# Optimization experiments

Measured on AMD Instinct MI355X. Metric: run time of the kernel, lower is better.

Reference implementation:

```python
import jax, jax.numpy as jnp
import numpy as np
import math

# geometry: ROI [-140.8,-40,-3,140.8,40,1], grid 0.4 -> (Z,Y,X)=(10,200,704)
B_AG = 2              # total agents = 1 sample x 2 agents
Z, Y, X = 10, 200, 704
Z1, Y1, X1 = 5, 100, 352   # after stride-2 conv (k=3, p=1)
N_PTS = 10000         # active radar voxels per agent
C_IN, C0, C1 = 64, 32, 64
N_IN = B_AG * N_PTS
CAP0 = 27 * N_IN                # padded bound on spconv0 active outputs
CAP1 = B_AG * Z1 * Y1 * X1      # padded bound on spconv1 active outputs
EPS = 1e-5

_OFFS = np.array([[a, b, c] for a in range(3) for b in range(3) for c in range(3)])


def _spconv_rulebook(coords, stride, zyx, pair_cap, out_cap):
    """Rulebook for SparseConv3d k=3 pad=1. coords [N,4]=(b,z,y,x).
    Returns gather [27,P], scatter [27,P] (dummy=out_cap), out coords padded
    to out_cap (pad coords are out-of-bounds so dense scatter drops them)."""
    oz, oy, ox = zyx
    per_in, per_lin = [], []
    for off in _OFFS:
        t = coords[:, 1:] + 1 - off
        ok = (t % stride == 0).all(1)
        o = t // stride
        ok &= (o >= 0).all(1) & (o[:, 0] < oz) & (o[:, 1] < oy) & (o[:, 2] < ox)
        idx = np.nonzero(ok)[0]
        oc = o[idx]
        per_in.append(idx)
        per_lin.append(((coords[idx, 0] * oz + oc[:, 0]) * oy + oc[:, 1]) * ox + oc[:, 2])
    all_lin = np.unique(np.concatenate(per_lin))
    n_out = len(all_lin)
    g = np.zeros((27, pair_cap), np.int32)
    s = np.full((27, pair_cap), out_cap, np.int32)
    for k in range(27):
        n = len(per_in[k])
        g[k, :n] = per_in[k]
        s[k, :n] = np.searchsorted(all_lin, per_lin[k])
    b = all_lin // (oz * oy * ox); r = all_lin % (oz * oy * ox)
    zc = r // (oy * ox); r = r % (oy * ox)
    out_coords = np.stack([b, zc, r // ox, r % ox], 1).astype(np.int32)
    pad = np.zeros((out_cap - n_out, 4), np.int32); pad[:, 1] = oz  # OOB -> dropped
    return g, s, np.concatenate([out_coords, pad], 0), n_out


def _subm_rulebook(coords, n_act, zyx, pair_cap, out_cap):
    """SubMConv3d k=3: same active set in/out; coords[:n_act] sorted by lin id."""
    oz, oy, ox = zyx
    c = coords[:n_act]
    lins = ((c[:, 0] * oz + c[:, 1]) * oy + c[:, 2]) * ox + c[:, 3]
    g = np.zeros((27, pair_cap), np.int32)
    s = np.full((27, pair_cap), out_cap, np.int32)
    for k, off in enumerate(_OFFS):
        cand = c[:, 1:] + (off - 1)
        ok = (cand >= 0).all(1) & (cand[:, 0] < oz) & (cand[:, 1] < oy) & (cand[:, 2] < ox)
        cl = ((c[:, 0] * oz + cand[:, 0]) * oy + cand[:, 1]) * ox + cand[:, 2]
        pos = np.minimum(np.searchsorted(lins, cl), n_act - 1)
        ok &= lins[pos] == cl
        idx = np.nonzero(ok)[0]
        g[k, :len(idx)] = pos[idx]
        s[k, :len(idx)] = idx
    return g, s


def setup_inputs() -> dict:
    rng = np.random.default_rng(0)
    cl = []
    for b in range(B_AG):
        lin = np.sort(rng.choice(Z * Y * X, N_PTS, replace=False))
        z = lin // (Y * X); r = lin % (Y * X)
        cl.append(np.stack([np.full(N_PTS, b), z, r // X, r % X], 1))
    coords_in = np.concatenate(cl, 0).astype(np.int64)

    g0, s0, coords0, n0 = _spconv_rulebook(coords_in, 1, (Z, Y, X), N_IN, CAP0)
    ga, sa = _subm_rulebook(coords0, n0, (Z, Y, X), CAP0, CAP0)
    g1, s1, coords1, n1 = _spconv_rulebook(coords0[:n0], 2, (Z1, Y1, X1), CAP0, CAP1)
    gb, sb = _subm_rulebook(coords1, n1, (Z1, Y1, X1), CAP1, CAP1)

    ks = jax.random.split(jax.random.key(0), 20)
    f32 = jnp.float32
    def W(k, *shape, fan):
        return jax.random.normal(k, shape, f32) * (1.0 / np.sqrt(fan))
    def bn(k, c):  # [gamma, beta, running_mean, running_var]
        m = jax.random.normal(k, (c,), f32) * 0.1
        v = 1.0 + jax.random.uniform(jax.random.fold_in(k, 1), (c,), f32)
        return jnp.stack([jnp.ones((c,), f32), jnp.zeros((c,), f32), m, v])
    return dict(
        sp_feats=jax.random.normal(ks[0], (N_IN, C_IN), f32),
        w_in=W(ks[1], C_IN, C0, fan=C_IN),
        w0=W(ks[2], 27, C0, C0, fan=27 * C0), bnp0=bn(ks[3], C0),
        w0a=W(ks[4], 27, C0, C0, fan=27 * C0), bnp0a=bn(ks[5], C0),
        w0b=W(ks[6], 27, C0, C0, fan=27 * C0), bnp0b=bn(ks[7], C0),
        w1=W(ks[8], 27, C0, C1, fan=27 * C0), bnp1=bn(ks[9], C1),
        w1a=W(ks[10], 27, C1, C1, fan=27 * C1), bnp1a=bn(ks[11], C1),
        w1b=W(ks[12], 27, C1, C1, fan=27 * C1), bnp1b=bn(ks[13], C1),
        ct0_w=W(ks[14], C0 * Z, 64, 1, 1, fan=C0 * Z), ct0_b=jnp.zeros((64,), f32),
        bnt0=bn(ks[15], 64),
        ct1_w=W(ks[16], C1 * Z1, 64, 2, 2, fan=C1 * Z1 * 4), ct1_b=jnp.zeros((64,), f32),
        bnt1=bn(ks[17], 64),
        coords0=jnp.asarray(coords0), coords1=jnp.asarray(coords1),
        g0=jnp.asarray(g0), s0=jnp.asarray(s0),
        ga=jnp.asarray(ga), sa=jnp.asarray(sa),
        g1=jnp.asarray(g1), s1=jnp.asarray(s1),
        gb=jnp.asarray(gb), sb=jnp.asarray(sb),
        record_len=2,
    )


def _bn1d(x, p):  # x [N,C]; p [4,C]
    g, b, m, v = p
    return (x - m) * (g * jax.lax.rsqrt(v + EPS)) + b


def _bn2d(x, p):  # x [B,C,H,W]
    g, b, m, v = (t[:, None, None] for t in p)
    return (x - m) * (g * jax.lax.rsqrt(v + EPS)) + b


def _spconv(feats, g, s, W, out_cap):
    """gather-GEMM-scatter: feats [Nin,Cin], g/s [27,P], W [27,Cin,Cout]."""
    out = jnp.zeros((out_cap + 1, W.shape[2]), feats.dtype)  # +1 dummy row
    for k in range(27):
        out = out.at[s[k]].add(feats[g[k]] @ W[k])
    return out[:out_cap]


def _to_dense(feats, coords, b, z, y, x):
    d = jnp.zeros((b, z, y, x, feats.shape[1]), feats.dtype)
    d = d.at[coords[:, 0], coords[:, 1], coords[:, 2], coords[:, 3]].add(feats)
    return d.transpose(0, 4, 1, 2, 3)  # B,C,Z,Y,X


def _conv_t2d(x, w, b, stride, pad):
    """torch ConvTranspose2d; w [Cin,Cout,k,k]."""
    k = w.shape[2]
    wf = jnp.flip(w, (2, 3)).transpose(1, 0, 2, 3)  # Cout,Cin,k,k
    out = jax.lax.conv_general_dilated(
        x, wf, window_strides=(1, 1),
        padding=[(k - 1 - pad, k - 1 - pad)] * 2,
        lhs_dilation=(stride, stride),
        dimension_numbers=('NCHW', 'OIHW', 'NCHW'))
    return out + b[None, :, None, None]


def _att_fusion(x, L):
    """OpenCOOD AttFusion: per-pixel scaled dot-product attention over agents,
    keep ego (agent 0). Assumes uniform record_len == L."""
    B, C, H, Wd = x.shape
    S = B // L
    xr = x.reshape(S, L, C, H * Wd).transpose(0, 3, 1, 2)  # S,HW,L,C
    att = jax.nn.softmax(jnp.einsum('snlc,snmc->snlm', xr, xr) / math.sqrt(C), -1)
    h = jnp.einsum('snlm,snmc->snlc', att, xr)[:, :, 0, :]  # ego agent
    return h.transpose(0, 2, 1).reshape(S, C, H, Wd)


def reference(sp_feats, w_in, w0, bnp0, w0a, bnp0a, w0b, bnp0b,
              w1, bnp1, w1a, bnp1a, w1b, bnp1b,
              ct0_w, ct0_b, bnt0, ct1_w, ct1_b, bnt1,
              coords0, coords1, g0, s0, ga, sa, g1, s1, gb, sb, record_len):
    relu = jax.nn.relu
    f = sp_feats @ w_in                         # input_conv (k=1)
    # ---- encoder layer 0 (stride 1) ----
    f = relu(_bn1d(_spconv(f, g0, s0, w0, CAP0), bnp0))
    f = relu(_bn1d(_spconv(f, ga, sa, w0a, CAP0), bnp0a))
    f = relu(_bn1d(_spconv(f, ga, sa, w0b, CAP0), bnp0b))
    d0 = _to_dense(f, coords0, B_AG, Z, Y, X).reshape(B_AG, C0 * Z, Y, X)  # b (c z) y x
    bev0 = relu(_bn2d(_conv_t2d(d0, ct0_w, ct0_b, 1, 0), bnt0))
    bev0 = _att_fusion(bev0, record_len)
    # ---- encoder layer 1 (stride 2) ----
    f = relu(_bn1d(_spconv(f, g1, s1, w1, CAP1), bnp1))
    f = relu(_bn1d(_spconv(f, gb, sb, w1a, CAP1), bnp1a))
    f = relu(_bn1d(_spconv(f, gb, sb, w1b, CAP1), bnp1b))
    d1 = _to_dense(f, coords1, B_AG, Z1, Y1, X1).reshape(B_AG, C1 * Z1, Y1, X1)
    bev1 = relu(_bn2d(_conv_t2d(d1, ct1_w, ct1_b, 2, 0), bnt1))
    bev1 = _att_fusion(bev1, record_len)
    return jnp.concatenate([bev0, bev1], axis=1)  # [S, 128, 200, 704]
```

## Files before the change

kernel.cpp:

```cpp
#include <hip/hip_runtime.h>
#include <hip/hip_bf16.h>
#include <hip/hip_fp16.h>

#define N_PTS_IN   20000
#define CAP0C      540000
#define CAP1C      352000
#define ZD 10
#define YD 200
#define XD 704
#define Z1D 5
#define Y1D 100
#define X1D 352
#define HWOUT (YD*XD)

typedef _Float16 f16x8 __attribute__((ext_vector_type(8)));
typedef float    f32x4 __attribute__((ext_vector_type(4)));

__global__ __launch_bounds__(256) void gemm_in(const float* __restrict__ sp,
                                               const float* __restrict__ w,
                                               __half* __restrict__ fout) {
    int tid = blockIdx.x * 256 + threadIdx.x;
    int row = tid >> 3;
    int c4  = (tid & 7) * 4;
    if (row >= N_PTS_IN) return;
    float4 acc = {0.f, 0.f, 0.f, 0.f};
    const float* sr = sp + (size_t)row * 64;
#pragma unroll
    for (int ci = 0; ci < 64; ci += 4) {
        float4 fv = *(const float4*)(sr + ci);
        const float* wp = w + ci * 32 + c4;
        float4 w0 = *(const float4*)(wp);
        float4 w1 = *(const float4*)(wp + 32);
        float4 w2 = *(const float4*)(wp + 64);
        float4 w3 = *(const float4*)(wp + 96);
        acc.x += fv.x*w0.x + fv.y*w1.x + fv.z*w2.x + fv.w*w3.x;
        acc.y += fv.x*w0.y + fv.y*w1.y + fv.z*w2.y + fv.w*w3.y;
        acc.z += fv.x*w0.z + fv.y*w1.z + fv.z*w2.z + fv.w*w3.z;
        acc.w += fv.x*w0.w + fv.y*w1.w + fv.z*w2.w + fv.w*w3.w;
    }
    __half* fo = fout + (size_t)row * 32 + c4;
    fo[0] = __float2half(acc.x);
    fo[1] = __float2half(acc.y);
    fo[2] = __float2half(acc.z);
    fo[3] = __float2half(acc.w);
}

__global__ __launch_bounds__(256) void cvt_w(const float* __restrict__ src,
                                             __half* __restrict__ dst,
                                             int CIN, int COUT) {
    int i = blockIdx.x * 256 + threadIdx.x;
    if (i >= 27 * CIN * COUT) return;
    int ci = i % CIN;
    int t  = i / CIN;
    int co = t % COUT;
    int k  = t / COUT;
    dst[i] = __float2half(src[((size_t)k * CIN + ci) * COUT + co]);
}

__global__ __launch_bounds__(256) void cvt_ct0(const float* __restrict__ src,
                                               __half* __restrict__ dst) {
    int i = blockIdx.x * 256 + threadIdx.x;
    if (i >= 64 * 320) return;
    int zc = i % 320, co = i / 320;
    int z = zc >> 5, c = zc & 31;
    dst[i] = __float2half(src[(c * 10 + z) * 64 + co]);
}

__global__ __launch_bounds__(256) void cvt_ct1(const float* __restrict__ src,
                                               __half* __restrict__ dst) {
    int i = blockIdx.x * 256 + threadIdx.x;
    if (i >= 4 * 64 * 320) return;
    int zc = i % 320;
    int t  = i / 320;
    int co = t & 63;
    int kq = t >> 6;
    int z = zc >> 6, c = zc & 63;
    dst[i] = __float2half(src[((c * 5 + z) * 64 + co) * 4 + kq]);
}

__global__ __launch_bounds__(256) void build_nbr(const int* __restrict__ g,
                                                 const int* __restrict__ s,
                                                 int* __restrict__ nbrT,
                                                 int P, int cap) {
    int i = blockIdx.x * 256 + threadIdx.x;
    if (i >= 27 * P) return;
    int k = i / P, p = i - k * P;
    int sv = s[(size_t)k * P + p];
    if (sv >= cap) return;
    nbrT[(size_t)k * cap + sv] = g[(size_t)k * P + p];
}

__global__ __launch_bounds__(128) void find_nact(const int* __restrict__ c0,
                                                 const int* __restrict__ c1,
                                                 int* __restrict__ nA) {
    int t = threadIdx.x;
    if (t == 0) {
        int lo = 0, hi = CAP0C;
        while (lo < hi) {
            int mid = (lo + hi) >> 1;
            if (c0[4 * mid + 1] >= ZD) hi = mid; else lo = mid + 1;
        }
        nA[0] = lo;
    } else if (t == 64) {
        int lo = 0, hi = CAP1C;
        while (lo < hi) {
            int mid = (lo + hi) >> 1;
            if (c1[4 * mid + 1] >= Z1D) hi = mid; else lo = mid + 1;
        }
        nA[1] = lo;
    }
}

__global__ __launch_bounds__(256) void build_vox(const int* __restrict__ coords,
                                                 int* __restrict__ v2r,
                                                 int cap, int Zdim, int Ydim, int Xdim) {
    int r = blockIdx.x * 256 + threadIdx.x;
    if (r >= cap) return;
    int b = coords[4*r], z = coords[4*r+1], y = coords[4*r+2], x = coords[4*r+3];
    if (z >= Zdim) return;
    v2r[(((size_t)b * Zdim + z) * Ydim + y) * Xdim + x] = r;
}

template <int CIN, int COUT>
__global__ __launch_bounds__(256) void spconv_reg(const __half* __restrict__ f,
                                                  const __half* __restrict__ wt,
                                                  const float* __restrict__ bnp,
                                                  const int* __restrict__ nbrT,
                                                  __half* __restrict__ fout,
                                                  int ncap,
                                                  const int* __restrict__ nA) {
    constexpr int NT = COUT / 16;
    constexpr int KT = CIN / 32;
    constexpr int NCHUNK = CIN / 8;
    constexpr int MASK = NCHUNK - 1;
    constexpr int LCH  = (NCHUNK == 8) ? 3 : 2;
    constexpr int TILE_H = COUT * CIN;
    constexpr int TB = TILE_H * 2 / 256;
    constexpr int OST_H = 4 * 32 * COUT;
    constexpr int SH_H = (2 * TILE_H > OST_H) ? 2 * TILE_H : OST_H;
    __shared__ __align__(16) __half S[SH_H];

    int tid = threadIdx.x;
    int wv = tid >> 6, lane = tid & 63;
    int quad = lane >> 4, l16 = lane & 15;

    int bid = blockIdx.x;
    int nfull = (int)gridDim.x & ~63;
    int sb;
    if (bid < nfull) {
        int grp = bid >> 6, w = bid & 63;
        sb = grp * 64 + (w & 7) * 8 + (w >> 3);
    } else {
        sb = bid;
    }

    if (sb * 128 >= *nA) return;

    int m0 = sb * 128 + wv * 32;
    int r0 = m0 + l16;
    int r1 = m0 + 16 + l16;
    bool ok0 = r0 < ncap, ok1 = r1 < ncap;

    f32x4 acc[2][NT] = {};

    int gC0 = ok0 ? nbrT[r0] : -1;
    int gC1 = ok1 ? nbrT[r1] : -1;
    int gN0 = ok0 ? nbrT[(size_t)ncap + r0] : -1;
    int gN1 = ok1 ? nbrT[(size_t)ncap + r1] : -1;
    bool ever = false;

    {
        const char* src = (const char*)(wt) + tid * TB;
        if constexpr (TB == 32) {
            uint4 w0 = *(const uint4*)src;
            uint4 w1 = *(const uint4*)(src + 16);
            int p0 = tid * 2;
#pragma unroll
            for (int j = 0; j < 2; ++j) {
                int p = p0 + j;
                int row = p >> LCH, c = p & MASK;
                *(uint4*)(S + (row * NCHUNK + (c ^ (row & MASK))) * 8) = (j ? w1 : w0);
            }
        } else if constexpr (TB == 16) {
            uint4 w0 = *(const uint4*)src;
            int p = tid;
            int row = p >> LCH, c = p & MASK;
            *(uint4*)(S + (row * NCHUNK + (c ^ (row & MASK))) * 8) = w0;
        } else {
            uint2 w0 = *(const uint2*)src;
            int p = tid >> 1, half = tid & 1;
            int row = p >> LCH, c = p & MASK;
            *(uint2*)(S + (row * NCHUNK + (c ^ (row & MASK))) * 8 + half * 4) = w0;
        }
    }
    __syncthreads();

#pragma unroll 1
    for (int k = 0; k < 27; ++k) {
        int gNN0 = -1, gNN1 = -1;
        if (k + 2 < 27) {
            if (ok0) gNN0 = nbrT[(size_t)(k + 2) * ncap + r0];
            if (ok1) gNN1 = nbrT[(size_t)(k + 2) * ncap + r1];
        }
        bool anyC = __ballot((gC0 >= 0) || (gC1 >= 0)) != 0ull;
        f16x8 a0[KT], a1[KT];
        if (anyC) {
            const __half* p0 = f + (size_t)((gC0 < 0) ? 0 : gC0) * CIN + quad * 8;
            const __half* p1 = f + (size_t)((gC1 < 0) ? 0 : gC1) * CIN + quad * 8;
#pragma unroll
            for (int kt = 0; kt < KT; ++kt) {
                uint4 u0 = {0u,0u,0u,0u}, u1 = {0u,0u,0u,0u};
                if (gC0 >= 0) u0 = *(const uint4*)(p0 + kt * 32);
                if (gC1 >= 0) u1 = *(const uint4*)(p1 + kt * 32);
                a0[kt] = *(f16x8*)&u0;
                a1[kt] = *(f16x8*)&u1;
            }
        }
        bool doStage = (k + 1 < 27);
        uint4 w0{}, w1{}; uint2 w2{};
        if (doStage) {
            const char* src = (const char*)(wt + (size_t)(k + 1) * TILE_H) + tid * TB;
            if constexpr (TB == 32)      { w0 = *(const uint4*)src; w1 = *(const uint4*)(src + 16); }
            else if constexpr (TB == 16) { w0 = *(const uint4*)src; }
            else                         { w2 = *(const uint2*)src; }
        }
        if (anyC) {
            ever = true;
            const __half* Wb = S + (k & 1) * TILE_H;
#pragma unroll
            for (int kt = 0; kt < KT; ++kt) {
#pragma unroll
                for (int nt = 0; nt < NT; ++nt) {
                    int row = nt * 16 + l16;
                    int c   = kt * 4 + quad;
                    f16x8 b = *(const f16x8*)(Wb + (row * NCHUNK + (c ^ (row & MASK))) * 8);
                    acc[0][nt] = __builtin_amdgcn_mfma_f32_16x16x32_f16(a0[kt], b, acc[0][nt], 0, 0, 0);
                    acc[1][nt] = __builtin_amdgcn_mfma_f32_16x16x32_f16(a1[kt], b, acc[1][nt], 0, 0, 0);
                }
            }
        }
        if (doStage) {
            __half* dst = S + ((k + 1) & 1) * TILE_H;
            if constexpr (TB == 32) {
                int p0 = tid * 2;
#pragma unroll
                for (int j = 0; j < 2; ++j) {
                    int p = p0 + j;
                    int row = p >> LCH, c = p & MASK;
                    *(uint4*)(dst + (row * NCHUNK + (c ^ (row & MASK))) * 8) = (j ? w1 : w0);
                }
            } else if constexpr (TB == 16) {
                int p = tid;
                int row = p >> LCH, c = p & MASK;
                *(uint4*)(dst + (row * NCHUNK + (c ^ (row & MASK))) * 8) = w0;
            } else {
                int p = tid >> 1, half = tid & 1;
                int row = p >> LCH, c = p & MASK;
                *(uint2*)(dst + (row * NCHUNK + (c ^ (row & MASK))) * 8 + half * 4) = w2;
            }
        }
        __syncthreads();
        gC0 = gN0; gC1 = gN1; gN0 = gNN0; gN1 = gNN1;
    }

    if (!ever) return;
    __half* O = S + wv * (32 * COUT);
#pragma unroll
    for (int nt = 0; nt < NT; ++nt) {
        int co = nt * 16 + l16;
        float g = bnp[co], b = bnp[COUT + co];
        float mn = bnp[2*COUT + co], vv = bnp[3*COUT + co];
        float s  = g * rsqrtf(vv + 1e-5f);
        float sh = b - mn * s;
#pragma unroll
        for (int m = 0; m < 2; ++m)
#pragma unroll
            for (int r_ = 0; r_ < 4; ++r_) {
                int row = m * 16 + quad * 4 + r_;
                O[row * COUT + co] = __float2half(fmaxf(acc[m][nt][r_] * s + sh, 0.f));
            }
    }
    constexpr int OCH = COUT / 8;
#pragma unroll
    for (int j = 0; j < 32 * OCH / 64; ++j) {
        int idx = j * 64 + lane;
        int r = idx / OCH, c = idx % OCH;
        if (m0 + r < ncap)
            *(uint4*)(fout + (size_t)(m0 + r) * COUT + c * 8) =
                *(const uint4*)(O + r * COUT + c * 8);
    }
}

__global__ __launch_bounds__(256) void bev0_mfma(const __half* __restrict__ f0,
                                                 const __half* __restrict__ wtT,
                                                 const float* __restrict__ bias,
                                                 const float* __restrict__ bnp,
                                                 const int* __restrict__ v2r,
                                                 float* __restrict__ out) {
    constexpr int AST = 328;
    __shared__ __align__(16) __half Al[64 * AST];
    __shared__ float Cl[64][65];
    __shared__ float Ot[64][33];
    int tid = threadIdx.x;
    int y = blockIdx.x / 22, x0 = (blockIdx.x % 22) * 32;
    int wv = tid >> 6, lane = tid & 63;
    int quad = lane >> 4, l16 = lane & 15;

    for (int it = 0; it < 3; ++it) {
        int task = it * 256 + tid;
        if (task < 640) {
            int row = task & 63, z = task >> 6;
            int b = row & 1, p = row >> 1;
            int r = v2r[((b * ZD + z) * YD + y) * XD + x0 + p];
            uint4 v0 = {0,0,0,0}, v1 = {0,0,0,0}, v2 = {0,0,0,0}, v3 = {0,0,0,0};
            if (r >= 0) {
                const uint4* src = (const uint4*)(f0 + (size_t)r * 32);
                v0 = src[0]; v1 = src[1]; v2 = src[2]; v3 = src[3];
            }
            uint4* dst = (uint4*)(Al + row * AST + z * 32);
            dst[0] = v0; dst[1] = v1; dst[2] = v2; dst[3] = v3;
        }
    }
    __syncthreads();

    f32x4 acc[4] = {};
#pragma unroll
    for (int ks = 0; ks < 10; ++ks) {
        f16x8 a = *(const f16x8*)(Al + (wv * 16 + l16) * AST + ks * 32 + quad * 8);
#pragma unroll
        for (int nt = 0; nt < 4; ++nt) {
            f16x8 bfr = *(const f16x8*)(wtT + (size_t)(nt * 16 + l16) * 320 + ks * 32 + quad * 8);
            acc[nt] = __builtin_amdgcn_mfma_f32_16x16x32_f16(a, bfr, acc[nt], 0, 0, 0);
        }
    }
#pragma unroll
    for (int nt = 0; nt < 4; ++nt) {
        int co = nt * 16 + l16;
        float s  = bnp[co] * rsqrtf(bnp[192 + co] + 1e-5f);
        float sh = (bias[co] - bnp[128 + co]) * s + bnp[64 + co];
#pragma unroll
        for (int r_ = 0; r_ < 4; ++r_)
            Cl[wv * 16 + quad * 4 + r_][co] = fmaxf(acc[nt][r_] * s + sh, 0.f);
    }
#pragma unroll
    for (int pi = 0; pi < 8; ++pi) {
        int p = wv * 8 + pi;
        float x0v = Cl[2 * p][lane], x1v = Cl[2 * p + 1][lane];
        float s00 = x0v * x0v, s01 = x0v * x1v;
#pragma unroll
        for (int o = 32; o > 0; o >>= 1) {
            s00 += __shfl_xor(s00, o);
            s01 += __shfl_xor(s01, o);
        }
        float a0 = s00 * 0.125f, a1 = s01 * 0.125f;
        float mx = fmaxf(a0, a1);
        float e0 = expf(a0 - mx), e1 = expf(a1 - mx);
        float inv = 1.f / (e0 + e1);
        Ot[lane][p] = (e0 * x0v + e1 * x1v) * inv;
    }
    __syncthreads();
#pragma unroll
    for (int i = 0; i < 8; ++i) {
        int idx = i * 256 + tid;
        int co = idx >> 5, px = idx & 31;
        out[(size_t)co * HWOUT + (size_t)y * XD + x0 + px] = Ot[co][px];
    }
}

__global__ __launch_bounds__(256) void bev1_mfma(const __half* __restrict__ f1,
                                                 const __half* __restrict__ wtT,
                                                 const float* __restrict__ bias,
                                                 const float* __restrict__ bnp,
                                                 const int* __restrict__ v2r,
                                                 float* __restrict__ out) {
    constexpr int AST = 328;
    __shared__ __align__(16) __half Al[64 * AST];
    __shared__ float Cl[64][65];
    __shared__ float Ot[64][65];
    int tid = threadIdx.x;
    int iy = blockIdx.x / 11, j0 = (blockIdx.x % 11) * 32;
    int wv = tid >> 6, lane = tid & 63;
    int quad = lane >> 4, l16 = lane & 15;

    for (int it = 0; it < 3; ++it) {
        int task = it * 256 + tid;
        if (task < 640) {
            int row = task & 63, zh = task >> 6;
            int z = zh >> 1, hf = zh & 1;
            int b = row & 1, p = row >> 1;
            int r = v2r[((b * Z1D + z) * Y1D + iy) * X1D + j0 + p];
            uint4 v0 = {0,0,0,0}, v1 = {0,0,0,0}, v2 = {0,0,0,0}, v3 = {0,0,0,0};
            if (r >= 0) {
                const uint4* src = (const uint4*)(f1 + (size_t)r * 64 + hf * 32);
                v0 = src[0]; v1 = src[1]; v2 = src[2]; v3 = src[3];
            }
            uint4* dst = (uint4*)(Al + row * AST + z * 64 + hf * 32);
            dst[0] = v0; dst[1] = v1; dst[2] = v2; dst[3] = v3;
        }
    }
    __syncthreads();

#pragma unroll 1
    for (int ky = 0; ky < 2; ++ky) {
#pragma unroll 1
        for (int kx = 0; kx < 2; ++kx) {
            const __half* wk = wtT + (size_t)(ky * 2 + kx) * 64 * 320;
            f32x4 acc[4] = {};
#pragma unroll
            for (int ks = 0; ks < 10; ++ks) {
                f16x8 a = *(const f16x8*)(Al + (wv * 16 + l16) * AST + ks * 32 + quad * 8);
#pragma unroll
                for (int nt = 0; nt < 4; ++nt) {
                    f16x8 bfr = *(const f16x8*)(wk + (size_t)(nt * 16 + l16) * 320 + ks * 32 + quad * 8);
                    acc[nt] = __builtin_amdgcn_mfma_f32_16x16x32_f16(a, bfr, acc[nt], 0, 0, 0);
                }
            }
#pragma unroll
            for (int nt = 0; nt < 4; ++nt) {
                int co = nt * 16 + l16;
                float s  = bnp[co] * rsqrtf(bnp[192 + co] + 1e-5f);
                float sh = (bias[co] - bnp[128 + co]) * s + bnp[64 + co];
#pragma unroll
                for (int r_ = 0; r_ < 4; ++r_)
                    Cl[wv * 16 + quad * 4 + r_][co] = fmaxf(acc[nt][r_] * s + sh, 0.f);
            }
#pragma unroll
            for (int pi = 0; pi < 8; ++pi) {
                int p = wv * 8 + pi;
                float x0v = Cl[2 * p][lane], x1v = Cl[2 * p + 1][lane];
                float s00 = x0v * x0v, s01 = x0v * x1v;
#pragma unroll
                for (int o = 32; o > 0; o >>= 1) {
                    s00 += __shfl_xor(s00, o);
                    s01 += __shfl_xor(s01, o);
                }
                float a0 = s00 * 0.125f, a1 = s01 * 0.125f;
                float mx = fmaxf(a0, a1);
                float e0 = expf(a0 - mx), e1 = expf(a1 - mx);
                float inv = 1.f / (e0 + e1);
                Ot[lane][2 * p + kx] = (e0 * x0v + e1 * x1v) * inv;
            }
        }
        __syncthreads();
        int yo = 2 * iy + ky;
#pragma unroll
        for (int i = 0; i < 16; ++i) {
            int idx = i * 256 + tid;
            int co = idx >> 6, xx = idx & 63;
            out[(size_t)co * HWOUT + (size_t)yo * XD + 2 * j0 + xx] = Ot[co][xx];
        }
        __syncthreads();
    }
}

extern "C" void kernel_launch(void* const* d_in, const int* in_sizes, int n_in,
                              void* d_out, int out_size, void* d_ws, size_t ws_size,
                              hipStream_t stream) {
    const float* sp    = (const float*)d_in[0];
    const float* w_in  = (const float*)d_in[1];
    const float* w0    = (const float*)d_in[2];
    const float* bnp0  = (const float*)d_in[3];
    const float* w0a   = (const float*)d_in[4];
    const float* bnp0a = (const float*)d_in[5];
    const float* w0b   = (const float*)d_in[6];
    const float* bnp0b = (const float*)d_in[7];
    const float* w1    = (const float*)d_in[8];
    const float* bnp1  = (const float*)d_in[9];
    const float* w1a   = (const float*)d_in[10];
    const float* bnp1a = (const float*)d_in[11];
    const float* w1b   = (const float*)d_in[12];
    const float* bnp1b = (const float*)d_in[13];
    const float* ct0w  = (const float*)d_in[14];
    const float* ct0b  = (const float*)d_in[15];
    const float* bnt0  = (const float*)d_in[16];
    const float* ct1w  = (const float*)d_in[17];
    const float* ct1b  = (const float*)d_in[18];
    const float* bnt1  = (const float*)d_in[19];
    const int* coords0 = (const int*)d_in[20];
    const int* coords1 = (const int*)d_in[21];
    const int* g0 = (const int*)d_in[22];
    const int* s0 = (const int*)d_in[23];
    const int* ga = (const int*)d_in[24];
    const int* sa = (const int*)d_in[25];
    const int* g1 = (const int*)d_in[26];
    const int* s1 = (const int*)d_in[27];
    const int* gb = (const int*)d_in[28];
    const int* sb = (const int*)d_in[29];
    float* out = (float*)d_out;

    __half* fInH = (__half*)d_ws;
    __half* R1h  = fInH + 640000;
    __half* R2h  = R1h + 22528000;
    __half* wt0  = R2h + 22528000;
    __half* wt0a = wt0  + 27648;
    __half* wt0b = wt0a + 27648;
    __half* wt1  = wt0b + 27648;
    __half* wt1a = wt1  + 55296;
    __half* wt1b = wt1a + 110592;
    __half* wtT0 = wt1b + 110592;
    __half* wtT1 = wtT0 + 20480;
    int*   nbrT = (int*)(wtT1 + 81920);
    int*   v2r0 = nbrT;
    int*   v2r1 = nbrT + 2816000;
    int*   nAct = nbrT + 14580000;

    find_nact<<<1, 128, 0, stream>>>(coords0, coords1, nAct);
    cvt_w<<<(27*32*32 + 255) / 256, 256, 0, stream>>>(w0,  wt0,  32, 32);
    cvt_w<<<(27*32*32 + 255) / 256, 256, 0, stream>>>(w0a, wt0a, 32, 32);
    cvt_w<<<(27*32*32 + 255) / 256, 256, 0, stream>>>(w0b, wt0b, 32, 32);
    cvt_w<<<(27*32*64 + 255) / 256, 256, 0, stream>>>(w1,  wt1,  32, 64);
    cvt_w<<<(27*64*64 + 255) / 256, 256, 0, stream>>>(w1a, wt1a, 64, 64);
    cvt_w<<<(27*64*64 + 255) / 256, 256, 0, stream>>>(w1b, wt1b, 64, 64);
    cvt_ct0<<<(64*320 + 255) / 256, 256, 0, stream>>>(ct0w, wtT0);
    cvt_ct1<<<(4*64*320 + 255) / 256, 256, 0, stream>>>(ct1w, wtT1);

    gemm_in<<<(N_PTS_IN * 8 + 255) / 256, 256, 0, stream>>>(sp, w_in, fInH);

    hipMemsetAsync(nbrT, 0xFF, (size_t)CAP0C * 27 * 4, stream);
    build_nbr<<<(27 * N_PTS_IN + 255) / 256, 256, 0, stream>>>(g0, s0, nbrT, N_PTS_IN, CAP0C);
    spconv_reg<32, 32><<<(CAP0C + 127) / 128, 256, 0, stream>>>(fInH, wt0, bnp0, nbrT, R1h, CAP0C, nAct + 0);

    hipMemsetAsync(nbrT, 0xFF, (size_t)CAP0C * 27 * 4, stream);
    build_nbr<<<(27 * CAP0C + 255) / 256, 256, 0, stream>>>(ga, sa, nbrT, CAP0C, CAP0C);
    spconv_reg<32, 32><<<(CAP0C + 127) / 128, 256, 0, stream>>>(R1h, wt0a, bnp0a, nbrT, R2h, CAP0C, nAct + 0);
    spconv_reg<32, 32><<<(CAP0C + 127) / 128, 256, 0, stream>>>(R2h, wt0b, bnp0b, nbrT, R1h, CAP0C, nAct + 0);

    hipMemsetAsync(v2r0, 0xFF, (size_t)2816000 * 4, stream);
    build_vox<<<(CAP0C + 255) / 256, 256, 0, stream>>>(coords0, v2r0, CAP0C, ZD, YD, XD);
    bev0_mfma<<<YD * 22, 256, 0, stream>>>(R1h, wtT0, ct0b, bnt0, v2r0, out);

    hipMemsetAsync(nbrT, 0xFF, (size_t)CAP1C * 27 * 4, stream);
    build_nbr<<<(27 * CAP0C + 255) / 256, 256, 0, stream>>>(g1, s1, nbrT, CAP0C, CAP1C);
    spconv_reg<32, 64><<<(CAP1C + 127) / 128, 256, 0, stream>>>(R1h, wt1, bnp1, nbrT, R2h, CAP1C, nAct + 1);

    hipMemsetAsync(nbrT, 0xFF, (size_t)CAP1C * 27 * 4, stream);
    build_nbr<<<(27 * CAP1C + 255) / 256, 256, 0, stream>>>(gb, sb, nbrT, CAP1C, CAP1C);
    spconv_reg<64, 64><<<(CAP1C + 127) / 128, 256, 0, stream>>>(R2h, wt1a, bnp1a, nbrT, R1h, CAP1C, nAct + 1);
    spconv_reg<64, 64><<<(CAP1C + 127) / 128, 256, 0, stream>>>(R1h, wt1b, bnp1b, nbrT, R2h, CAP1C, nAct + 1);

    hipMemsetAsync(v2r1, 0xFF, (size_t)352000 * 4, stream);
    build_vox<<<(CAP1C + 255) / 256, 256, 0, stream>>>(coords1, v2r1, CAP1C, Z1D, Y1D, X1D);
    bev1_mfma<<<Y1D * 11, 256, 0, stream>>>(R2h, wtT1, ct1b, bnt1, v2r1, out + (size_t)64 * HWOUT);
}
```

Baseline: 1.024 ms.

## Load BEV conv A-operands directly into registers and fuse attention in-register

Result: faster. 977.2 us (-4.6%).

```diff
diff --git a/kernel.cpp b/kernel.cpp
--- a/kernel.cpp
+++ b/kernel.cpp
@@ -297,72 +297,85 @@
                                                  const float* __restrict__ bnp,
                                                  const int* __restrict__ v2r,
                                                  float* __restrict__ out) {
-    constexpr int AST = 328;
-    __shared__ __align__(16) __half Al[64 * AST];
-    __shared__ float Cl[64][65];
-    __shared__ float Ot[64][33];
+    __shared__ float Ot[64][66];
     int tid = threadIdx.x;
-    int y = blockIdx.x / 22, x0 = (blockIdx.x % 22) * 32;
+    int y = blockIdx.x / 11, x0 = (blockIdx.x % 11) * 64;
     int wv = tid >> 6, lane = tid & 63;
     int quad = lane >> 4, l16 = lane & 15;
 
-    for (int it = 0; it < 3; ++it) {
-        int task = it * 256 + tid;
-        if (task < 640) {
-            int row = task & 63, z = task >> 6;
-            int b = row & 1, p = row >> 1;
-            int r = v2r[((b * ZD + z) * YD + y) * XD + x0 + p];
-            uint4 v0 = {0,0,0,0}, v1 = {0,0,0,0}, v2 = {0,0,0,0}, v3 = {0,0,0,0};
-            if (r >= 0) {
-                const uint4* src = (const uint4*)(f0 + (size_t)r * 32);
-                v0 = src[0]; v1 = src[1]; v2 = src[2]; v3 = src[3];
-            }
-            uint4* dst = (uint4*)(Al + row * AST + z * 32);
-            dst[0] = v0; dst[1] = v1; dst[2] = v2; dst[3] = v3;
-        }
-    }
-    __syncthreads();
-
-    f32x4 acc[4] = {};
+    int rz[2][10];
+#pragma unroll
+    for (int m = 0; m < 2; ++m) {
+        int row = wv * 32 + m * 16 + l16;
+        int b = row & 1, p = row >> 1;
+#pragma unroll
+        for (int z = 0; z < 10; ++z)
+            rz[m][z] = v2r[((b * ZD + z) * YD + y) * XD + x0 + p];
+    }
+
+    f32x4 acc[2][4] = {};
 #pragma unroll
     for (int ks = 0; ks < 10; ++ks) {
-        f16x8 a = *(const f16x8*)(Al + (wv * 16 + l16) * AST + ks * 32 + quad * 8);
+        f16x8 a[2];
+#pragma unroll
+        for (int m = 0; m < 2; ++m) {
+            uint4 u = {0u,0u,0u,0u};
+            int r = rz[m][ks];
+            if (r >= 0) u = *(const uint4*)(f0 + (size_t)r * 32 + quad * 8);
+            a[m] = *(f16x8*)&u;
+        }
 #pragma unroll
         for (int nt = 0; nt < 4; ++nt) {
-            f16x8 bfr = *(const f16x8*)(wtT + (size_t)(nt * 16 + l16) * 320 + ks * 32 + quad * 8);
-            acc[nt] = __builtin_amdgcn_mfma_f32_16x16x32_f16(a, bfr, acc[nt], 0, 0, 0);
-        }
-    }
+            f16x8 b = *(const f16x8*)(wtT + (size_t)(nt * 16 + l16) * 320 + ks * 32 + quad * 8);
+            acc[0][nt] = __builtin_amdgcn_mfma_f32_16x16x32_f16(a[0], b, acc[0][nt], 0, 0, 0);
+            acc[1][nt] = __builtin_amdgcn_mfma_f32_16x16x32_f16(a[1], b, acc[1][nt], 0, 0, 0);
+        }
+    }
+
 #pragma unroll
     for (int nt = 0; nt < 4; ++nt) {
         int co = nt * 16 + l16;
         float s  = bnp[co] * rsqrtf(bnp[192 + co] + 1e-5f);
         float sh = (bias[co] - bnp[128 + co]) * s + bnp[64 + co];
 #pragma unroll
-        for (int r_ = 0; r_ < 4; ++r_)
-            Cl[wv * 16 + quad * 4 + r_][co] = fmaxf(acc[nt][r_] * s + sh, 0.f);
-    }
-#pragma unroll
-    for (int pi = 0; pi < 8; ++pi) {
-        int p = wv * 8 + pi;
-        float x0v = Cl[2 * p][lane], x1v = Cl[2 * p + 1][lane];
-        float s00 = x0v * x0v, s01 = x0v * x1v;
-#pragma unroll
-        for (int o = 32; o > 0; o >>= 1) {
-            s00 += __shfl_xor(s00, o);
-            s01 += __shfl_xor(s01, o);
-        }
-        float a0 = s00 * 0.125f, a1 = s01 * 0.125f;
-        float mx = fmaxf(a0, a1);
-        float e0 = expf(a0 - mx), e1 = expf(a1 - mx);
-        float inv = 1.f / (e0 + e1);
-        Ot[lane][p] = (e0 * x0v + e1 * x1v) * inv;
-    }
+        for (int m = 0; m < 2; ++m)
+#pragma unroll
+            for (int r_ = 0; r_ < 4; ++r_)
+                acc[m][nt][r_] = fmaxf(acc[m][nt][r_] * s + sh, 0.f);
+    }
+
+#pragma unroll
+    for (int m = 0; m < 2; ++m)
+#pragma unroll
+        for (int jj = 0; jj < 2; ++jj) {
+            float s00 = 0.f, s01 = 0.f;
+#pragma unroll
+            for (int nt = 0; nt < 4; ++nt) {
+                float xv0 = acc[m][nt][2 * jj], xv1 = acc[m][nt][2 * jj + 1];
+                s00 += xv0 * xv0;
+                s01 += xv0 * xv1;
+            }
+#pragma unroll
+            for (int o = 8; o > 0; o >>= 1) {
+                s00 += __shfl_xor(s00, o);
+                s01 += __shfl_xor(s01, o);
+            }
+            float a0 = s00 * 0.125f, a1 = s01 * 0.125f;
+            float mx = fmaxf(a0, a1);
+            float e0 = expf(a0 - mx), e1 = expf(a1 - mx);
+            float inv = 1.f / (e0 + e1);
+            int pl = wv * 16 + m * 8 + quad * 2 + jj;
+#pragma unroll
+            for (int nt = 0; nt < 4; ++nt)
+                Ot[nt * 16 + l16][pl] =
+                    (e0 * acc[m][nt][2 * jj] + e1 * acc[m][nt][2 * jj + 1]) * inv;
+        }
     __syncthreads();
-#pragma unroll
-    for (int i = 0; i < 8; ++i) {
+
+#pragma unroll
+    for (int i = 0; i < 16; ++i) {
         int idx = i * 256 + tid;
-        int co = idx >> 5, px = idx & 31;
+        int co = idx >> 6, px = idx & 63;
         out[(size_t)co * HWOUT + (size_t)y * XD + x0 + px] = Ot[co][px];
     }
 }
@@ -373,32 +386,18 @@
                                                  const float* __restrict__ bnp,
                                                  const int* __restrict__ v2r,
                                                  float* __restrict__ out) {
-    constexpr int AST = 328;
-    __shared__ __align__(16) __half Al[64 * AST];
-    __shared__ float Cl[64][65];
-    __shared__ float Ot[64][65];
+    __shared__ float Ot[64][66];
     int tid = threadIdx.x;
     int iy = blockIdx.x / 11, j0 = (blockIdx.x % 11) * 32;
     int wv = tid >> 6, lane = tid & 63;
     int quad = lane >> 4, l16 = lane & 15;
 
-    for (int it = 0; it < 3; ++it) {
-        int task = it * 256 + tid;
-        if (task < 640) {
-            int row = task & 63, zh = task >> 6;
-            int z = zh >> 1, hf = zh & 1;
-            int b = row & 1, p = row >> 1;
-            int r = v2r[((b * Z1D + z) * Y1D + iy) * X1D + j0 + p];
-            uint4 v0 = {0,0,0,0}, v1 = {0,0,0,0}, v2 = {0,0,0,0}, v3 = {0,0,0,0};
-            if (r >= 0) {
-                const uint4* src = (const uint4*)(f1 + (size_t)r * 64 + hf * 32);
-                v0 = src[0]; v1 = src[1]; v2 = src[2]; v3 = src[3];
-            }
-            uint4* dst = (uint4*)(Al + row * AST + z * 64 + hf * 32);
-            dst[0] = v0; dst[1] = v1; dst[2] = v2; dst[3] = v3;
-        }
-    }
-    __syncthreads();
+    int row = wv * 16 + l16;
+    int b = row & 1, p = row >> 1;
+    int rz[5];
+#pragma unroll
+    for (int z = 0; z < 5; ++z)
+        rz[z] = v2r[((b * Z1D + z) * Y1D + iy) * X1D + j0 + p];
 
 #pragma unroll 1
     for (int ky = 0; ky < 2; ++ky) {
@@ -408,11 +407,15 @@
             f32x4 acc[4] = {};
 #pragma unroll
             for (int ks = 0; ks < 10; ++ks) {
-                f16x8 a = *(const f16x8*)(Al + (wv * 16 + l16) * AST + ks * 32 + quad * 8);
+                int z = ks >> 1, hf = ks & 1;
+                uint4 u = {0u,0u,0u,0u};
+                int r = rz[z];
+                if (r >= 0) u = *(const uint4*)(f1 + (size_t)r * 64 + hf * 32 + quad * 8);
+                f16x8 a = *(f16x8*)&u;
 #pragma unroll
                 for (int nt = 0; nt < 4; ++nt) {
-                    f16x8 bfr = *(const f16x8*)(wk + (size_t)(nt * 16 + l16) * 320 + ks * 32 + quad * 8);
-                    acc[nt] = __builtin_amdgcn_mfma_f32_16x16x32_f16(a, bfr, acc[nt], 0, 0, 0);
+                    f16x8 bf = *(const f16x8*)(wk + (size_t)(nt * 16 + l16) * 320 + ks * 32 + quad * 8);
+                    acc[nt] = __builtin_amdgcn_mfma_f32_16x16x32_f16(a, bf, acc[nt], 0, 0, 0);
                 }
             }
 #pragma unroll
@@ -422,15 +425,19 @@
                 float sh = (bias[co] - bnp[128 + co]) * s + bnp[64 + co];
 #pragma unroll
                 for (int r_ = 0; r_ < 4; ++r_)
-                    Cl[wv * 16 + quad * 4 + r_][co] = fmaxf(acc[nt][r_] * s + sh, 0.f);
-            }
-#pragma unroll
-            for (int pi = 0; pi < 8; ++pi) {
-                int p = wv * 8 + pi;
-                float x0v = Cl[2 * p][lane], x1v = Cl[2 * p + 1][lane];
-                float s00 = x0v * x0v, s01 = x0v * x1v;
-#pragma unroll
-                for (int o = 32; o > 0; o >>= 1) {
+                    acc[nt][r_] = fmaxf(acc[nt][r_] * s + sh, 0.f);
+            }
+#pragma unroll
+            for (int jj = 0; jj < 2; ++jj) {
+                float s00 = 0.f, s01 = 0.f;
+#pragma unroll
+                for (int nt = 0; nt < 4; ++nt) {
+                    float xv0 = acc[nt][2 * jj], xv1 = acc[nt][2 * jj + 1];
+                    s00 += xv0 * xv0;
+                    s01 += xv0 * xv1;
+                }
+#pragma unroll
+                for (int o = 8; o > 0; o >>= 1) {
                     s00 += __shfl_xor(s00, o);
                     s01 += __shfl_xor(s01, o);
                 }
@@ -438,7 +445,11 @@
                 float mx = fmaxf(a0, a1);
                 float e0 = expf(a0 - mx), e1 = expf(a1 - mx);
                 float inv = 1.f / (e0 + e1);
-                Ot[lane][2 * p + kx] = (e0 * x0v + e1 * x1v) * inv;
+                int pl = wv * 8 + quad * 2 + jj;
+#pragma unroll
+                for (int nt = 0; nt < 4; ++nt)
+                    Ot[nt * 16 + l16][2 * pl + kx] =
+                        (e0 * acc[nt][2 * jj] + e1 * acc[nt][2 * jj + 1]) * inv;
             }
         }
         __syncthreads();
@@ -527,7 +538,7 @@
 
     hipMemsetAsync(v2r0, 0xFF, (size_t)2816000 * 4, stream);
     build_vox<<<(CAP0C + 255) / 256, 256, 0, stream>>>(coords0, v2r0, CAP0C, ZD, YD, XD);
-    bev0_mfma<<<YD * 22, 256, 0, stream>>>(R1h, wtT0, ct0b, bnt0, v2r0, out);
+    bev0_mfma<<<YD * 11, 256, 0, stream>>>(R1h, wtT0, ct0b, bnt0, v2r0, out);
 
     hipMemsetAsync(nbrT, 0xFF, (size_t)CAP1C * 27 * 4, stream);
     build_nbr<<<(27 * CAP0C + 255) / 256, 256, 0, stream>>>(g1, s1, nbrT, CAP0C, CAP1C);
```
